# Kernel tuning notes

Hardware: AMD Instinct MI355X
Metric: run time of the kernel (lower is better)

## Reference

```python
import jax, jax.numpy as jnp
import numpy as np

N_NODES = 100000
N_EDGES = 3200000


def gcn_conv(x, edge_index, W, b, n_nodes):
    # PyG GCNConv: x' = D^{-1/2} (A + I) D^{-1/2} (x W) + b
    h = x @ W  # [N, C_out]
    loop = jnp.arange(n_nodes, dtype=edge_index.dtype)
    src = jnp.concatenate([edge_index[0], loop])  # source nodes j
    dst = jnp.concatenate([edge_index[1], loop])  # target nodes i (aggregation)
    deg = jax.ops.segment_sum(jnp.ones_like(dst, h.dtype), dst, num_segments=n_nodes)
    dinv = jnp.where(deg > 0, jax.lax.rsqrt(deg), 0.0)
    norm = dinv[src] * dinv[dst]  # [E+N]
    msg = h[src] * norm[:, None]  # gather + scale
    out = jax.ops.segment_sum(msg, dst, num_segments=n_nodes)  # scatter-add
    return out + b


def setup_inputs() -> dict:
    key = jax.random.key(0)
    ks = jax.random.split(key, 6)
    x = jax.random.normal(ks[0], (N_NODES, 1), dtype=jnp.float32)
    edge_index = jax.random.randint(ks[1], (2, N_EDGES), 0, N_NODES, dtype=jnp.int64)
    W1 = jax.random.normal(ks[2], (1, 16), dtype=jnp.float32) * (1.0 / np.sqrt(1))
    b1 = jnp.zeros((16,), dtype=jnp.float32)
    W2 = jax.random.normal(ks[3], (16, 16), dtype=jnp.float32) * (1.0 / np.sqrt(16))
    b2 = jnp.zeros((16,), dtype=jnp.float32)
    Wl = jax.random.normal(ks[4], (16, 1), dtype=jnp.float32) * (1.0 / np.sqrt(16))
    bl = jnp.zeros((1,), dtype=jnp.float32)
    return {"x": x, "edge_index": edge_index, "W1": W1, "b1": b1,
            "W2": W2, "b2": b2, "Wl": Wl, "bl": bl}


def reference(x, edge_index, W1, b1, W2, b2, Wl, bl):
    n = x.shape[0]
    h = gcn_conv(x, edge_index, W1, b1, n)
    h = jax.nn.relu(h)
    # F.dropout(training=self.training): identity in eval mode
    h = gcn_conv(h, edge_index, W2, b2, n)
    return h @ Wl + bl  # [N, 1]
```

## Files before the change

kernel.cpp:

```cpp
#include <hip/hip_runtime.h>

#define N_NODES  100000
#define N_EDGES  3200000
#define NB       8
#define BN       12544
#define BNH      (BN / 2)
#define NRT      256
#define NDG      64
#define DSL      8
#define THR      1024
#define QPB      (N_EDGES / NRT / 4)
#define QDS      (N_EDGES / DSL / 4)
#define CAP      2048
#define SA       32
#define SPS      (NRT / SA)
#define GA       (NB * SA)
#define TRD      256


__global__ __launch_bounds__(THR) void k_route_deg(
        const int* __restrict__ ei, unsigned* __restrict__ cnt,
        unsigned* __restrict__ pedge, unsigned* __restrict__ pdeg) {
    __shared__ __align__(16) unsigned smem[BN];
    __shared__ unsigned bcnt[NB], bbase[NB], bcur[NB];
    const int tid = threadIdx.x;
    const uint4* d4 = (const uint4*)(ei + N_EDGES);

    if (blockIdx.x < NDG) {
        const int bu = blockIdx.x >> 3, s = blockIdx.x & 7;
        for (int i = tid; i < BNH; i += THR) smem[i] = 0u;
        __syncthreads();
        const unsigned base_node = (unsigned)bu * BN;
        const int q1 = (s + 1) * QDS;
        #pragma unroll 2
        for (int q = s * QDS + tid; q < q1; q += THR) {
            const uint4 dv = d4[q];
            const unsigned dd[4] = { dv.x, dv.y, dv.z, dv.w };
            #pragma unroll
            for (int k = 0; k < 4; ++k) {
                const unsigned d = dd[k];
                if (d / BN == (unsigned)bu) {
                    const unsigned dl = d - base_node;
                    atomicAdd(&smem[dl >> 1], 1u << ((dl & 1) << 4));
                }
            }
        }
        __syncthreads();
        uint4* po = (uint4*)(pdeg + (size_t)blockIdx.x * BNH);
        const uint4* fi = (const uint4*)smem;
        for (int i = tid; i < BNH / 4; i += THR) po[i] = fi[i];
        return;
    }

    const int blk = blockIdx.x - NDG;
    if (tid < NB) bcnt[tid] = 0u;
    __syncthreads();

    const uint4* s4 = (const uint4*)ei;
    const int q0 = blk * QPB;
    uint4 dq[4], sq[4];
    #pragma unroll
    for (int i = 0; i < 4; ++i) {
        const int q = tid + i * THR;
        if (q < QPB) { dq[i] = d4[q0 + q]; sq[i] = s4[q0 + q]; }
    }

    unsigned c01 = 0, c23 = 0;
    #pragma unroll
    for (int i = 0; i < 4; ++i) {
        const int q = tid + i * THR;
        if (q < QPB) {
            const unsigned dd[4] = { dq[i].x, dq[i].y, dq[i].z, dq[i].w };
            #pragma unroll
            for (int k = 0; k < 4; ++k) {
                const unsigned b = dd[k] / BN;
                if (b < 4) c01 += 1u << (8 * b);
                else       c23 += 1u << (8 * (b - 4));
            }
        }
    }
    #pragma unroll
    for (int b = 0; b < 4; ++b) {
        const unsigned v0 = (c01 >> (8 * b)) & 0xFFu;
        const unsigned v1 = (c23 >> (8 * b)) & 0xFFu;
        if (v0) atomicAdd(&bcnt[b], v0);
        if (v1) atomicAdd(&bcnt[b + 4], v1);
    }
    __syncthreads();
    if (tid == 0) {
        unsigned run = 0;
        #pragma unroll
        for (int b = 0; b < NB; ++b) { bbase[b] = run; bcur[b] = run; run += bcnt[b]; }
    }
    __syncthreads();

    #pragma unroll
    for (int i = 0; i < 4; ++i) {
        const int q = tid + i * THR;
        if (q < QPB) {
            const unsigned dd[4] = { dq[i].x, dq[i].y, dq[i].z, dq[i].w };
            const unsigned ss[4] = { sq[i].x, sq[i].y, sq[i].z, sq[i].w };
            #pragma unroll
            for (int k = 0; k < 4; ++k) {
                const unsigned d = dd[k];
                const unsigned b = d / BN;
                const unsigned slot = atomicAdd(&bcur[b], 1u);
                smem[slot] = ss[k] | ((d - b * BN) << 17);
            }
        }
    }
    __syncthreads();

    #pragma unroll
    for (int b = 0; b < NB; ++b) {
        const unsigned n = bcnt[b] < CAP ? bcnt[b] : CAP;
        const unsigned base = bbase[b];
        unsigned* reg = pedge + ((size_t)(blk * NB + b)) * CAP;
        for (unsigned j = tid; j < n; j += THR) reg[j] = smem[base + j];
    }
    if (tid < NB) cnt[blk * NB + tid] = bcnt[tid] < CAP ? bcnt[tid] : CAP;
}

__global__ __launch_bounds__(THR) void k_acc(
        const unsigned* __restrict__ pedge, const unsigned* __restrict__ cnt,
        const float* __restrict__ vals, float* __restrict__ partials) {
    __shared__ __align__(16) float facc[BN];
    const int tid = threadIdx.x;
    const int bu = blockIdx.x / SA, sub = blockIdx.x % SA;
    for (int i = tid; i < BN / 4; i += THR)
        ((float4*)facc)[i] = make_float4(0.f, 0.f, 0.f, 0.f);
    __syncthreads();
    for (int s = 0; s < SPS; ++s) {
        const int r = (sub * SPS + s) * NB + bu;
        const unsigned n = cnt[r];
        const unsigned* reg = pedge + (size_t)r * CAP;
        const uint4* reg4 = (const uint4*)reg;
        const unsigned n4 = n >> 2;
        for (unsigned j = tid; j < n4; j += THR) {
            const uint4 w = reg4[j];
            const float v0 = vals[w.x & 0x1FFFFu];
            const float v1 = vals[w.y & 0x1FFFFu];
            const float v2 = vals[w.z & 0x1FFFFu];
            const float v3 = vals[w.w & 0x1FFFFu];
            atomicAdd(&facc[w.x >> 17], v0);
            atomicAdd(&facc[w.y >> 17], v1);
            atomicAdd(&facc[w.z >> 17], v2);
            atomicAdd(&facc[w.w >> 17], v3);
        }
        for (unsigned j = (n4 << 2) + tid; j < n; j += THR) {
            const unsigned w = reg[j];
            atomicAdd(&facc[w >> 17], vals[w & 0x1FFFFu]);
        }
    }
    __syncthreads();
    float4* po = (float4*)(partials + (size_t)blockIdx.x * BN);
    const float4* fi = (const float4*)facc;
    for (int i = tid; i < BN / 4; i += THR) po[i] = fi[i];
}

__device__ __forceinline__ float sum_partials(const float* __restrict__ partials,
                                              int g) {
    const int bu = g / BN, l = g - bu * BN;
    const float* pp = partials + (size_t)(bu * SA) * BN + l;
    float s = 0.f;
    #pragma unroll
    for (int k = 0; k < SA; ++k) s += pp[(size_t)k * BN];
    return s;
}

__global__ __launch_bounds__(TRD) void k_red1(const float* __restrict__ x,
        const unsigned* __restrict__ pdeg,
        float* __restrict__ dinv, float* __restrict__ xs) {
    const int t = blockIdx.x * TRD + threadIdx.x;
    const int g0 = 2 * t;
    if (g0 >= N_NODES) return;
    const int bu = g0 / BN, l = g0 - bu * BN;
    const unsigned* pp = pdeg + (size_t)(bu * DSL) * BNH + (l >> 1);
    unsigned r0 = 0, r1 = 0;
    #pragma unroll
    for (int s = 0; s < DSL; ++s) {
        const unsigned w = pp[(size_t)s * BNH];
        r0 += w & 0xFFFFu; r1 += w >> 16;
    }
    const float di0 = rsqrtf((float)r0 + 1.f);
    const float di1 = rsqrtf((float)r1 + 1.f);
    const float2 xv = *(const float2*)(x + g0);
    *(float2*)(dinv + g0) = make_float2(di0, di1);
    *(float2*)(xs + g0)   = make_float2(xv.x * di0, xv.y * di1);
}

__global__ __launch_bounds__(TRD) void k_red2(const float* __restrict__ x,
        const float* __restrict__ partials, const float* __restrict__ dinv,
        const float* __restrict__ W1, const float* __restrict__ b1,
        const float* __restrict__ W2, const float* __restrict__ Wl,
        float* __restrict__ us, float* __restrict__ uself) {
    const int g = blockIdx.x * TRD + threadIdx.x;
    if (g >= N_NODES) return;
    const float sum = sum_partials(partials, g);
    const float di = dinv[g];
    const float s1 = di * sum + x[g] * di * di;
    float u = 0.f;
    #pragma unroll
    for (int c = 0; c < 16; ++c) {
        float vcc = 0.f;
        #pragma unroll
        for (int k = 0; k < 16; ++k) vcc += W2[c * 16 + k] * Wl[k];
        u += fmaxf(W1[c] * s1 + b1[c], 0.f) * vcc;
    }
    us[g] = u * di;
    uself[g] = u * di * di;
}

__global__ __launch_bounds__(TRD) void k_red3(const float* __restrict__ partials,
        const float* __restrict__ dinv, const float* __restrict__ uself,
        const float* __restrict__ W2, const float* __restrict__ b2,
        const float* __restrict__ Wl, const float* __restrict__ bl,
        float* __restrict__ out) {
    const int g = blockIdx.x * TRD + threadIdx.x;
    if (g >= N_NODES) return;
    const float sum = sum_partials(partials, g);
    float vcb = bl[0];
    #pragma unroll
    for (int c = 0; c < 16; ++c) {
        float vcc = 0.f;
        #pragma unroll
        for (int k = 0; k < 16; ++k) vcc += W2[c * 16 + k] * Wl[k];
        vcb += b2[c] * vcc;
    }
    out[g] = dinv[g] * sum + uself[g] + vcb;
}

extern "C" void kernel_launch(void* const* d_in, const int* in_sizes, int n_in,
                              void* d_out, int out_size, void* d_ws, size_t ws_size,
                              hipStream_t stream) {
    const float* x  = (const float*)d_in[0];
    const int*   ei = (const int*)d_in[1];
    const float* W1 = (const float*)d_in[2];
    const float* b1 = (const float*)d_in[3];
    const float* W2 = (const float*)d_in[4];
    const float* b2 = (const float*)d_in[5];
    const float* Wl = (const float*)d_in[6];
    const float* bl = (const float*)d_in[7];
    float* out = (float*)d_out;

    unsigned* cnt      = (unsigned*)d_ws;
    unsigned* pedge    = cnt + NRT * NB;
    float*    partials = (float*)(pedge + (size_t)NRT * NB * CAP);
    unsigned* pdeg     = (unsigned*)(partials + (size_t)GA * BN);
    float*    dinv     = (float*)(pdeg + (size_t)NDG * BNH);
    float*    xs       = dinv + N_NODES;
    float*    us       = xs + N_NODES;
    float*    uself    = us + N_NODES;

    const int rb1 = (N_NODES / 2 + TRD - 1) / TRD;
    const int rb  = (N_NODES + TRD - 1) / TRD;

    k_route_deg<<<NDG + NRT, THR, 0, stream>>>(ei, cnt, pedge, pdeg);
    k_red1 <<<rb1, TRD, 0, stream>>>(x, pdeg, dinv, xs);
    k_acc  <<<GA,  THR, 0, stream>>>(pedge, cnt, xs, partials);
    k_red2 <<<rb,  TRD, 0, stream>>>(x, partials, dinv, W1, b1, W2, Wl, us, uself);
    k_acc  <<<GA,  THR, 0, stream>>>(pedge, cnt, us, partials);
    k_red3 <<<rb,  TRD, 0, stream>>>(partials, dinv, uself, W2, b2, Wl, bl, out);
}
```

Measured before the change: 189.6 us.

## Compute degrees from routed edge buckets and double accumulation-block split

Drops the separate degree-counting blocks that rescanned all destination indices in the routing kernel. Degrees are now counted by a new kernel that reads the already-bucketed packed edges and uses per-block shared-memory histograms, and pdeg reuses the partials buffer. The per-bucket block split SA goes from 32 to 64, and the accumulate loops now process two edge segments per iteration to expose more memory-level parallelism. The cost is an extra kernel launch and twice as many partial arrays to reduce in the reduction kernels.

```diff
diff --git a/kernel.cpp b/kernel.cpp
--- a/kernel.cpp
+++ b/kernel.cpp
@@ -6,57 +6,27 @@
 #define BN       12544
 #define BNH      (BN / 2)
 #define NRT      256
-#define NDG      64
-#define DSL      8
 #define THR      1024
 #define QPB      (N_EDGES / NRT / 4)
-#define QDS      (N_EDGES / DSL / 4)
 #define CAP      2048
-#define SA       32
+#define SA       64
 #define SPS      (NRT / SA)
 #define GA       (NB * SA)
 #define TRD      256
-
-
-__global__ __launch_bounds__(THR) void k_route_deg(
+#define M17      0x1FFFFu
+
+
+__global__ __launch_bounds__(THR) void k_route(
         const int* __restrict__ ei, unsigned* __restrict__ cnt,
-        unsigned* __restrict__ pedge, unsigned* __restrict__ pdeg) {
-    __shared__ __align__(16) unsigned smem[BN];
+        unsigned* __restrict__ pedge) {
+    __shared__ __align__(16) unsigned stag[BN];
     __shared__ unsigned bcnt[NB], bbase[NB], bcur[NB];
-    const int tid = threadIdx.x;
+    const int tid = threadIdx.x, blk = blockIdx.x;
+    if (tid < NB) bcnt[tid] = 0u;
+    __syncthreads();
+
+    const uint4* s4 = (const uint4*)ei;
     const uint4* d4 = (const uint4*)(ei + N_EDGES);
-
-    if (blockIdx.x < NDG) {
-        const int bu = blockIdx.x >> 3, s = blockIdx.x & 7;
-        for (int i = tid; i < BNH; i += THR) smem[i] = 0u;
-        __syncthreads();
-        const unsigned base_node = (unsigned)bu * BN;
-        const int q1 = (s + 1) * QDS;
-        #pragma unroll 2
-        for (int q = s * QDS + tid; q < q1; q += THR) {
-            const uint4 dv = d4[q];
-            const unsigned dd[4] = { dv.x, dv.y, dv.z, dv.w };
-            #pragma unroll
-            for (int k = 0; k < 4; ++k) {
-                const unsigned d = dd[k];
-                if (d / BN == (unsigned)bu) {
-                    const unsigned dl = d - base_node;
-                    atomicAdd(&smem[dl >> 1], 1u << ((dl & 1) << 4));
-                }
-            }
-        }
-        __syncthreads();
-        uint4* po = (uint4*)(pdeg + (size_t)blockIdx.x * BNH);
-        const uint4* fi = (const uint4*)smem;
-        for (int i = tid; i < BNH / 4; i += THR) po[i] = fi[i];
-        return;
-    }
-
-    const int blk = blockIdx.x - NDG;
-    if (tid < NB) bcnt[tid] = 0u;
-    __syncthreads();
-
-    const uint4* s4 = (const uint4*)ei;
     const int q0 = blk * QPB;
     uint4 dq[4], sq[4];
     #pragma unroll
@@ -105,7 +75,7 @@
                 const unsigned d = dd[k];
                 const unsigned b = d / BN;
                 const unsigned slot = atomicAdd(&bcur[b], 1u);
-                smem[slot] = ss[k] | ((d - b * BN) << 17);
+                stag[slot] = ss[k] | ((d - b * BN) << 17);
             }
         }
     }
@@ -116,41 +86,92 @@
         const unsigned n = bcnt[b] < CAP ? bcnt[b] : CAP;
         const unsigned base = bbase[b];
         unsigned* reg = pedge + ((size_t)(blk * NB + b)) * CAP;
-        for (unsigned j = tid; j < n; j += THR) reg[j] = smem[base + j];
+        for (unsigned j = tid; j < n; j += THR) reg[j] = stag[base + j];
     }
     if (tid < NB) cnt[blk * NB + tid] = bcnt[tid] < CAP ? bcnt[tid] : CAP;
 }
 
-__global__ __launch_bounds__(THR) void k_acc(
+__global__ __launch_bounds__(THR, 8) void k_accd(
+        const unsigned* __restrict__ pedge, const unsigned* __restrict__ cnt,
+        unsigned* __restrict__ pdeg) {
+    __shared__ __align__(16) unsigned ucnt[BN];
+    const int tid = threadIdx.x;
+    const int bu = blockIdx.x >> 6, sub = blockIdx.x & 63;
+    for (int i = tid; i < BN; i += THR) ucnt[i] = 0u;
+    __syncthreads();
+    #pragma unroll
+    for (int p = 0; p < SPS / 2; ++p) {
+        const int r0 = (sub * SPS + 2 * p)     * NB + bu;
+        const int r1 = (sub * SPS + 2 * p + 1) * NB + bu;
+        const unsigned n0 = cnt[r0], n1 = cnt[r1];
+        const uint4* g0 = (const uint4*)(pedge + (size_t)r0 * CAP);
+        const uint4* g1 = (const uint4*)(pedge + (size_t)r1 * CAP);
+        const unsigned q0 = n0 >> 2, q1 = n1 >> 2;
+        const unsigned m4 = q0 > q1 ? q0 : q1;
+        for (unsigned j = tid; j < m4; j += THR) {
+            if (j < q0) {
+                const uint4 w = g0[j];
+                atomicAdd(&ucnt[w.x >> 17], 1u); atomicAdd(&ucnt[w.y >> 17], 1u);
+                atomicAdd(&ucnt[w.z >> 17], 1u); atomicAdd(&ucnt[w.w >> 17], 1u);
+            }
+            if (j < q1) {
+                const uint4 w = g1[j];
+                atomicAdd(&ucnt[w.x >> 17], 1u); atomicAdd(&ucnt[w.y >> 17], 1u);
+                atomicAdd(&ucnt[w.z >> 17], 1u); atomicAdd(&ucnt[w.w >> 17], 1u);
+            }
+        }
+        const unsigned* e0 = (const unsigned*)g0;
+        for (unsigned j = (n0 & ~3u) + tid; j < n0; j += THR)
+            atomicAdd(&ucnt[e0[j] >> 17], 1u);
+        const unsigned* e1 = (const unsigned*)g1;
+        for (unsigned j = (n1 & ~3u) + tid; j < n1; j += THR)
+            atomicAdd(&ucnt[e1[j] >> 17], 1u);
+    }
+    __syncthreads();
+    unsigned* po = pdeg + (size_t)blockIdx.x * BNH;
+    for (int i = tid; i < BNH; i += THR)
+        po[i] = (ucnt[2 * i] & 0xFFFFu) | (ucnt[2 * i + 1] << 16);
+}
+
+__global__ __launch_bounds__(THR, 8) void k_acc(
         const unsigned* __restrict__ pedge, const unsigned* __restrict__ cnt,
         const float* __restrict__ vals, float* __restrict__ partials) {
     __shared__ __align__(16) float facc[BN];
     const int tid = threadIdx.x;
-    const int bu = blockIdx.x / SA, sub = blockIdx.x % SA;
+    const int bu = blockIdx.x >> 6, sub = blockIdx.x & 63;
     for (int i = tid; i < BN / 4; i += THR)
         ((float4*)facc)[i] = make_float4(0.f, 0.f, 0.f, 0.f);
     __syncthreads();
-    for (int s = 0; s < SPS; ++s) {
-        const int r = (sub * SPS + s) * NB + bu;
-        const unsigned n = cnt[r];
-        const unsigned* reg = pedge + (size_t)r * CAP;
-        const uint4* reg4 = (const uint4*)reg;
-        const unsigned n4 = n >> 2;
-        for (unsigned j = tid; j < n4; j += THR) {
-            const uint4 w = reg4[j];
-            const float v0 = vals[w.x & 0x1FFFFu];
-            const float v1 = vals[w.y & 0x1FFFFu];
-            const float v2 = vals[w.z & 0x1FFFFu];
-            const float v3 = vals[w.w & 0x1FFFFu];
-            atomicAdd(&facc[w.x >> 17], v0);
-            atomicAdd(&facc[w.y >> 17], v1);
-            atomicAdd(&facc[w.z >> 17], v2);
-            atomicAdd(&facc[w.w >> 17], v3);
-        }
-        for (unsigned j = (n4 << 2) + tid; j < n; j += THR) {
-            const unsigned w = reg[j];
-            atomicAdd(&facc[w >> 17], vals[w & 0x1FFFFu]);
-        }
+    #pragma unroll
+    for (int p = 0; p < SPS / 2; ++p) {
+        const int r0 = (sub * SPS + 2 * p)     * NB + bu;
+        const int r1 = (sub * SPS + 2 * p + 1) * NB + bu;
+        const unsigned n0 = cnt[r0], n1 = cnt[r1];
+        const uint4* g0 = (const uint4*)(pedge + (size_t)r0 * CAP);
+        const uint4* g1 = (const uint4*)(pedge + (size_t)r1 * CAP);
+        const unsigned q0 = n0 >> 2, q1 = n1 >> 2;
+        const unsigned m4 = q0 > q1 ? q0 : q1;
+        for (unsigned j = tid; j < m4; j += THR) {
+            const bool a0 = j < q0, a1 = j < q1;
+            uint4 w0, w1;
+            if (a0) w0 = g0[j];
+            if (a1) w1 = g1[j];
+            float v00, v01, v02, v03, v10, v11, v12, v13;
+            if (a0) { v00 = vals[w0.x & M17]; v01 = vals[w0.y & M17];
+                      v02 = vals[w0.z & M17]; v03 = vals[w0.w & M17]; }
+            if (a1) { v10 = vals[w1.x & M17]; v11 = vals[w1.y & M17];
+                      v12 = vals[w1.z & M17]; v13 = vals[w1.w & M17]; }
+            if (a0) { atomicAdd(&facc[w0.x >> 17], v00); atomicAdd(&facc[w0.y >> 17], v01);
+                      atomicAdd(&facc[w0.z >> 17], v02); atomicAdd(&facc[w0.w >> 17], v03); }
+            if (a1) { atomicAdd(&facc[w1.x >> 17], v10); atomicAdd(&facc[w1.y >> 17], v11);
+                      atomicAdd(&facc[w1.z >> 17], v12); atomicAdd(&facc[w1.w >> 17], v13); }
+        }
+        const unsigned* e0 = (const unsigned*)g0;
+        for (unsigned j = (n0 & ~3u) + tid; j < n0; j += THR)
+            atomicAdd(&facc[e0[j] >> 17], vals[e0[j] & M17]);
+        const unsigned* e1 = (const unsigned*)g1;
+        for (unsigned j = (n1 & ~3u) + tid; j < n1; j += THR)
+            atomicAdd(&facc[e1[j] >> 17], vals[e1[j] & M17]);
     }
     __syncthreads();
     float4* po = (float4*)(partials + (size_t)blockIdx.x * BN);
@@ -163,7 +184,7 @@
     const int bu = g / BN, l = g - bu * BN;
     const float* pp = partials + (size_t)(bu * SA) * BN + l;
     float s = 0.f;
-    #pragma unroll
+    #pragma unroll 16
     for (int k = 0; k < SA; ++k) s += pp[(size_t)k * BN];
     return s;
 }
@@ -175,10 +196,10 @@
     const int g0 = 2 * t;
     if (g0 >= N_NODES) return;
     const int bu = g0 / BN, l = g0 - bu * BN;
-    const unsigned* pp = pdeg + (size_t)(bu * DSL) * BNH + (l >> 1);
+    const unsigned* pp = pdeg + (size_t)(bu * SA) * BNH + (l >> 1);
     unsigned r0 = 0, r1 = 0;
-    #pragma unroll
-    for (int s = 0; s < DSL; ++s) {
+    #pragma unroll 16
+    for (int s = 0; s < SA; ++s) {
         const unsigned w = pp[(size_t)s * BNH];
         r0 += w & 0xFFFFu; r1 += w >> 16;
     }
@@ -246,8 +267,8 @@
     unsigned* cnt      = (unsigned*)d_ws;
     unsigned* pedge    = cnt + NRT * NB;
     float*    partials = (float*)(pedge + (size_t)NRT * NB * CAP);
-    unsigned* pdeg     = (unsigned*)(partials + (size_t)GA * BN);
-    float*    dinv     = (float*)(pdeg + (size_t)NDG * BNH);
+    unsigned* pdeg     = (unsigned*)partials;
+    float*    dinv     = partials + (size_t)GA * BN;
     float*    xs       = dinv + N_NODES;
     float*    us       = xs + N_NODES;
     float*    uself    = us + N_NODES;
@@ -255,7 +276,8 @@
     const int rb1 = (N_NODES / 2 + TRD - 1) / TRD;
     const int rb  = (N_NODES + TRD - 1) / TRD;
 
-    k_route_deg<<<NDG + NRT, THR, 0, stream>>>(ei, cnt, pedge, pdeg);
+    k_route<<<NRT, THR, 0, stream>>>(ei, cnt, pedge);
+    k_accd <<<GA,  THR, 0, stream>>>(pedge, cnt, pdeg);
     k_red1 <<<rb1, TRD, 0, stream>>>(x, pdeg, dinv, xs);
     k_acc  <<<GA,  THR, 0, stream>>>(pedge, cnt, xs, partials);
     k_red2 <<<rb,  TRD, 0, stream>>>(x, partials, dinv, W1, b1, W2, Wl, us, uself);
```

After: 190.8 us. Within noise of the previous version (+0.7%).

## Compute degrees with global atomics in router and double accumulator split

Applied to the files above, without the earlier changes.

Removes the dedicated degree-counting blocks, which re-read the destination array per bucket with packed 16-bit shared counters. Degrees are now counted with global atomics inside the routing kernel, after a memset of the degree array. The accumulation grid is also doubled (SA 32 to 64), so each block handles fewer routed segments, with an occupancy hint on k_acc. The trade-off is 3.2M contended global atomics plus twice as many partial buffers to write and reduce in the reduction kernels.

```diff
diff --git a/kernel.cpp b/kernel.cpp
--- a/kernel.cpp
+++ b/kernel.cpp
@@ -4,59 +4,28 @@
 #define N_EDGES  3200000
 #define NB       8
 #define BN       12544
-#define BNH      (BN / 2)
 #define NRT      256
-#define NDG      64
-#define DSL      8
 #define THR      1024
 #define QPB      (N_EDGES / NRT / 4)
-#define QDS      (N_EDGES / DSL / 4)
 #define CAP      2048
-#define SA       32
+#define SA       64
 #define SPS      (NRT / SA)
 #define GA       (NB * SA)
 #define TRD      256
-
-
-__global__ __launch_bounds__(THR) void k_route_deg(
+#define M17      0x1FFFFu
+
+
+__global__ __launch_bounds__(THR) void k_route(
         const int* __restrict__ ei, unsigned* __restrict__ cnt,
-        unsigned* __restrict__ pedge, unsigned* __restrict__ pdeg) {
-    __shared__ __align__(16) unsigned smem[BN];
+        unsigned* __restrict__ pedge, unsigned* __restrict__ deg) {
+    __shared__ __align__(16) unsigned stag[BN];
     __shared__ unsigned bcnt[NB], bbase[NB], bcur[NB];
-    const int tid = threadIdx.x;
+    const int tid = threadIdx.x, blk = blockIdx.x;
+    if (tid < NB) bcnt[tid] = 0u;
+    __syncthreads();
+
+    const uint4* s4 = (const uint4*)ei;
     const uint4* d4 = (const uint4*)(ei + N_EDGES);
-
-    if (blockIdx.x < NDG) {
-        const int bu = blockIdx.x >> 3, s = blockIdx.x & 7;
-        for (int i = tid; i < BNH; i += THR) smem[i] = 0u;
-        __syncthreads();
-        const unsigned base_node = (unsigned)bu * BN;
-        const int q1 = (s + 1) * QDS;
-        #pragma unroll 2
-        for (int q = s * QDS + tid; q < q1; q += THR) {
-            const uint4 dv = d4[q];
-            const unsigned dd[4] = { dv.x, dv.y, dv.z, dv.w };
-            #pragma unroll
-            for (int k = 0; k < 4; ++k) {
-                const unsigned d = dd[k];
-                if (d / BN == (unsigned)bu) {
-                    const unsigned dl = d - base_node;
-                    atomicAdd(&smem[dl >> 1], 1u << ((dl & 1) << 4));
-                }
-            }
-        }
-        __syncthreads();
-        uint4* po = (uint4*)(pdeg + (size_t)blockIdx.x * BNH);
-        const uint4* fi = (const uint4*)smem;
-        for (int i = tid; i < BNH / 4; i += THR) po[i] = fi[i];
-        return;
-    }
-
-    const int blk = blockIdx.x - NDG;
-    if (tid < NB) bcnt[tid] = 0u;
-    __syncthreads();
-
-    const uint4* s4 = (const uint4*)ei;
     const int q0 = blk * QPB;
     uint4 dq[4], sq[4];
     #pragma unroll
@@ -73,7 +42,9 @@
             const unsigned dd[4] = { dq[i].x, dq[i].y, dq[i].z, dq[i].w };
             #pragma unroll
             for (int k = 0; k < 4; ++k) {
-                const unsigned b = dd[k] / BN;
+                const unsigned d = dd[k];
+                atomicAdd(&deg[d], 1u);
+                const unsigned b = d / BN;
                 if (b < 4) c01 += 1u << (8 * b);
                 else       c23 += 1u << (8 * (b - 4));
             }
@@ -105,7 +76,7 @@
                 const unsigned d = dd[k];
                 const unsigned b = d / BN;
                 const unsigned slot = atomicAdd(&bcur[b], 1u);
-                smem[slot] = ss[k] | ((d - b * BN) << 17);
+                stag[slot] = ss[k] | ((d - b * BN) << 17);
             }
         }
     }
@@ -116,20 +87,21 @@
         const unsigned n = bcnt[b] < CAP ? bcnt[b] : CAP;
         const unsigned base = bbase[b];
         unsigned* reg = pedge + ((size_t)(blk * NB + b)) * CAP;
-        for (unsigned j = tid; j < n; j += THR) reg[j] = smem[base + j];
+        for (unsigned j = tid; j < n; j += THR) reg[j] = stag[base + j];
     }
     if (tid < NB) cnt[blk * NB + tid] = bcnt[tid] < CAP ? bcnt[tid] : CAP;
 }
 
-__global__ __launch_bounds__(THR) void k_acc(
+__global__ __launch_bounds__(THR, 8) void k_acc(
         const unsigned* __restrict__ pedge, const unsigned* __restrict__ cnt,
         const float* __restrict__ vals, float* __restrict__ partials) {
     __shared__ __align__(16) float facc[BN];
     const int tid = threadIdx.x;
-    const int bu = blockIdx.x / SA, sub = blockIdx.x % SA;
+    const int bu = blockIdx.x >> 6, sub = blockIdx.x & 63;
     for (int i = tid; i < BN / 4; i += THR)
         ((float4*)facc)[i] = make_float4(0.f, 0.f, 0.f, 0.f);
     __syncthreads();
+    #pragma unroll
     for (int s = 0; s < SPS; ++s) {
         const int r = (sub * SPS + s) * NB + bu;
         const unsigned n = cnt[r];
@@ -138,18 +110,18 @@
         const unsigned n4 = n >> 2;
         for (unsigned j = tid; j < n4; j += THR) {
             const uint4 w = reg4[j];
-            const float v0 = vals[w.x & 0x1FFFFu];
-            const float v1 = vals[w.y & 0x1FFFFu];
-            const float v2 = vals[w.z & 0x1FFFFu];
-            const float v3 = vals[w.w & 0x1FFFFu];
+            const float v0 = vals[w.x & M17];
+            const float v1 = vals[w.y & M17];
+            const float v2 = vals[w.z & M17];
+            const float v3 = vals[w.w & M17];
             atomicAdd(&facc[w.x >> 17], v0);
             atomicAdd(&facc[w.y >> 17], v1);
             atomicAdd(&facc[w.z >> 17], v2);
             atomicAdd(&facc[w.w >> 17], v3);
         }
-        for (unsigned j = (n4 << 2) + tid; j < n; j += THR) {
+        for (unsigned j = (n & ~3u) + tid; j < n; j += THR) {
             const unsigned w = reg[j];
-            atomicAdd(&facc[w >> 17], vals[w & 0x1FFFFu]);
+            atomicAdd(&facc[w >> 17], vals[w & M17]);
         }
     }
     __syncthreads();
@@ -163,27 +135,20 @@
     const int bu = g / BN, l = g - bu * BN;
     const float* pp = partials + (size_t)(bu * SA) * BN + l;
     float s = 0.f;
-    #pragma unroll
+    #pragma unroll 16
     for (int k = 0; k < SA; ++k) s += pp[(size_t)k * BN];
     return s;
 }
 
 __global__ __launch_bounds__(TRD) void k_red1(const float* __restrict__ x,
-        const unsigned* __restrict__ pdeg,
+        const unsigned* __restrict__ deg,
         float* __restrict__ dinv, float* __restrict__ xs) {
     const int t = blockIdx.x * TRD + threadIdx.x;
     const int g0 = 2 * t;
     if (g0 >= N_NODES) return;
-    const int bu = g0 / BN, l = g0 - bu * BN;
-    const unsigned* pp = pdeg + (size_t)(bu * DSL) * BNH + (l >> 1);
-    unsigned r0 = 0, r1 = 0;
-    #pragma unroll
-    for (int s = 0; s < DSL; ++s) {
-        const unsigned w = pp[(size_t)s * BNH];
-        r0 += w & 0xFFFFu; r1 += w >> 16;
-    }
-    const float di0 = rsqrtf((float)r0 + 1.f);
-    const float di1 = rsqrtf((float)r1 + 1.f);
+    const uint2 dv = *(const uint2*)(deg + g0);
+    const float di0 = rsqrtf((float)dv.x + 1.f);
+    const float di1 = rsqrtf((float)dv.y + 1.f);
     const float2 xv = *(const float2*)(x + g0);
     *(float2*)(dinv + g0) = make_float2(di0, di1);
     *(float2*)(xs + g0)   = make_float2(xv.x * di0, xv.y * di1);
@@ -246,8 +211,8 @@
     unsigned* cnt      = (unsigned*)d_ws;
     unsigned* pedge    = cnt + NRT * NB;
     float*    partials = (float*)(pedge + (size_t)NRT * NB * CAP);
-    unsigned* pdeg     = (unsigned*)(partials + (size_t)GA * BN);
-    float*    dinv     = (float*)(pdeg + (size_t)NDG * BNH);
+    unsigned* deg      = (unsigned*)(partials + (size_t)GA * BN);
+    float*    dinv     = (float*)(deg + N_NODES);
     float*    xs       = dinv + N_NODES;
     float*    us       = xs + N_NODES;
     float*    uself    = us + N_NODES;
@@ -255,8 +220,9 @@
     const int rb1 = (N_NODES / 2 + TRD - 1) / TRD;
     const int rb  = (N_NODES + TRD - 1) / TRD;
 
-    k_route_deg<<<NDG + NRT, THR, 0, stream>>>(ei, cnt, pedge, pdeg);
-    k_red1 <<<rb1, TRD, 0, stream>>>(x, pdeg, dinv, xs);
+    hipMemsetAsync(deg, 0, (size_t)N_NODES * sizeof(unsigned), stream);
+    k_route<<<NRT, THR, 0, stream>>>(ei, cnt, pedge, deg);
+    k_red1 <<<rb1, TRD, 0, stream>>>(x, deg, dinv, xs);
     k_acc  <<<GA,  THR, 0, stream>>>(pedge, cnt, xs, partials);
     k_red2 <<<rb,  TRD, 0, stream>>>(x, partials, dinv, W1, b1, W2, Wl, us, uself);
     k_acc  <<<GA,  THR, 0, stream>>>(pedge, cnt, us, partials);
```

Result: slower. 293.9 us (+55.1%).
